# Kernel optimization log

Measured on AMD Instinct MI355X. Metric: run time of the kernel, lower is better.

Reference implementation:

```python
import jax, jax.numpy as jnp
import numpy as np

N_NODES = 50000
N_EDGES = 800000
IN_DIM = 128
HID = 128
N_GRAPHS = 1024


def gcn_conv(x, W, b, src, dst, n_nodes):
    # PyG GCNConv: add self-loops, symmetric normalization, aggregate at dst, then bias.
    loop = jnp.arange(n_nodes, dtype=src.dtype)
    s = jnp.concatenate([src, loop])
    d = jnp.concatenate([dst, loop])
    deg = jax.ops.segment_sum(jnp.ones_like(d, dtype=x.dtype), d, num_segments=n_nodes)
    dinv = jnp.where(deg > 0, deg ** -0.5, 0.0)
    norm = dinv[s] * dinv[d]                      # [E+N]
    h = x @ W                                     # [N, out]
    msg = h[s] * norm[:, None]                    # gather + scale
    out = jax.ops.segment_sum(msg, d, num_segments=n_nodes)  # scatter-add
    return out + b


def setup_inputs() -> dict:
    key = jax.random.key(0)
    ks = jax.random.split(key, 10)
    x = jax.random.normal(ks[0], (N_NODES, IN_DIM), dtype=jnp.float32)
    src = jax.random.randint(ks[1], (N_EDGES,), 0, N_NODES, dtype=jnp.int32)
    dst = jax.random.randint(ks[2], (N_EDGES,), 0, N_NODES, dtype=jnp.int32)
    batch = jnp.sort(jax.random.randint(ks[3], (N_NODES,), 0, N_GRAPHS, dtype=jnp.int32))
    sc1 = 1.0 / np.sqrt(IN_DIM)
    sc2 = 1.0 / np.sqrt(HID)
    W1 = jax.random.uniform(ks[4], (IN_DIM, HID), jnp.float32, -sc1, sc1)
    b1 = jnp.zeros((HID,), jnp.float32)
    W2 = jax.random.uniform(ks[5], (HID, HID), jnp.float32, -sc2, sc2)
    b2 = jnp.zeros((HID,), jnp.float32)
    Wlin = jax.random.uniform(ks[6], (HID, 1), jnp.float32, -sc2, sc2)
    blin = jnp.zeros((1,), jnp.float32)
    return {"x": x, "src": src, "dst": dst, "batch": batch, "n_graphs": N_GRAPHS,
            "W1": W1, "b1": b1, "W2": W2, "b2": b2, "Wlin": Wlin, "blin": blin}


def reference(x, src, dst, batch, n_graphs, W1, b1, W2, b2, Wlin, blin):
    n = x.shape[0]
    h = jax.nn.relu(gcn_conv(x, W1, b1, src, dst, n))
    h = jax.nn.relu(gcn_conv(h, W2, b2, src, dst, n))
    # global_mean_pool over graph assignment
    summed = jax.ops.segment_sum(h, batch, num_segments=n_graphs)
    cnt = jax.ops.segment_sum(jnp.ones((n,), h.dtype), batch, num_segments=n_graphs)
    pooled = summed / jnp.maximum(cnt, 1.0)[:, None]
    return (pooled @ Wlin + blin).reshape(-1)
```

## Files before the change

### kernel.cpp

```cpp
#include <hip/hip_runtime.h>
#include <hip/hip_bf16.h>

#define DIM 128
typedef unsigned int u32;

typedef __attribute__((ext_vector_type(8))) short bf16x8;
typedef __attribute__((ext_vector_type(4))) float f32x4;
typedef __attribute__((ext_vector_type(2))) float f32x2;

__device__ __forceinline__ u32 pack_bf16x2(float a, float b) {
    u32 ua = __float_as_uint(a), ub = __float_as_uint(b);
    ua = (ua + 0x7FFFu + ((ua >> 16) & 1u)) >> 16;
    ub = (ub + 0x7FFFu + ((ub >> 16) & 1u)) >> 16;
    return ua | (ub << 16);
}
__device__ __forceinline__ float2 unpack_bf16x2(u32 h) {
    return make_float2(__uint_as_float(h << 16), __uint_as_float(h & 0xFFFF0000u));
}

#if __has_builtin(__builtin_amdgcn_cvt_pk_f32_fp8) && __has_builtin(__builtin_amdgcn_cvt_pk_fp8_f32)
#define FP8_HW 1
#endif

__device__ __forceinline__ void dec4(float* d, u32 w) {
#ifdef FP8_HW
    f32x2 a = __builtin_amdgcn_cvt_pk_f32_fp8((int)w, false);
    f32x2 b = __builtin_amdgcn_cvt_pk_f32_fp8((int)w, true);
    d[0] = a.x; d[1] = a.y; d[2] = b.x; d[3] = b.y;
#else
    #pragma unroll
    for (int i = 0; i < 4; ++i) {
        u32 v = (w >> (8 * i)) & 0xFFu;
        u32 s = v >> 7, e = (v >> 3) & 15u, m = v & 7u;
        float nv = __uint_as_float((s << 31) | ((e + 120u) << 23) | (m << 20));
        float sv = (s ? -1.f : 1.f) * (float)m * 0.001953125f;
        d[i] = e ? nv : sv;
    }
#endif
}

#ifndef FP8_HW
__device__ __forceinline__ u32 enc_byte(float f) {
    u32 s = __float_as_uint(f) >> 31;
    float af = fminf(fabsf(f), 448.f);
    u32 b;
    if (af >= 0.015625f) {
        u32 m = __float_as_uint(af);
        m = m + 0x0007FFFFu + ((m >> 20) & 1u);
        u32 fe = (m >> 23) - 120u;
        if (fe > 15u) b = (15u << 3) | 6u;
        else          b = (fe << 3) | ((m >> 20) & 7u);
    } else {
        b = (u32)rintf(af * 512.f);
    }
    return b | (s << 7);
}
#endif

template<bool HI>
__device__ __forceinline__ u32 enc_pair(float a, float b, u32 old) {
#ifdef FP8_HW
    return (u32)__builtin_amdgcn_cvt_pk_fp8_f32(a, b, (int)old, HI);
#else
    u32 p = enc_byte(a) | (enc_byte(b) << 8);
    return HI ? ((old & 0x0000FFFFu) | (p << 16)) : ((old & 0xFFFF0000u) | p);
#endif
}

__device__ __forceinline__ void addrow16(float* acc, uint4 r) {
    float d[4];
    dec4(d, r.x);
    acc[0]  += d[0]; acc[1]  += d[1]; acc[2]  += d[2]; acc[3]  += d[3];
    dec4(d, r.y);
    acc[4]  += d[0]; acc[5]  += d[1]; acc[6]  += d[2]; acc[7]  += d[3];
    dec4(d, r.z);
    acc[8]  += d[0]; acc[9]  += d[1]; acc[10] += d[2]; acc[11] += d[3];
    dec4(d, r.w);
    acc[12] += d[0]; acc[13] += d[1]; acc[14] += d[2]; acc[15] += d[3];
}

__global__ void count_rank(int* __restrict__ deg, const int* __restrict__ dst,
                           int* __restrict__ rank, int* __restrict__ total, int E)
{
    int e = blockIdx.x * blockDim.x + threadIdx.x;
    if (e == 0) *total = 0;
    if (e < E) rank[e] = atomicAdd(&deg[dst[e]], 1);
}

__global__ __launch_bounds__(256) void alloc_offsets(
    const int* __restrict__ deg, int* __restrict__ start, int* __restrict__ endp,
    float* __restrict__ dinv, int* __restrict__ total,
    int* __restrict__ csr, int N,
    float* __restrict__ sums, float* __restrict__ cnt, int G,
    u32* __restrict__ B0, u32* __restrict__ B1)
{
    int i = blockIdx.x * blockDim.x + threadIdx.x;
    int lane = threadIdx.x & 63;
    if (i < G) { sums[i] = 0.f; cnt[i] = 0.f; }
    if (i < 32) {
        B0[(size_t)N * 32 + i] = 0u;
        B1[(size_t)N * 32 + i] = 0u;
    }
    int d  = (i < N) ? deg[i] : 0;
    int d4 = (d + 3) & ~3;
    int pre = d4;
    #pragma unroll
    for (int off = 1; off < 64; off <<= 1) {
        int v = __shfl_up(pre, off, 64);
        if (lane >= off) pre += v;
    }
    int waveTot = __shfl(pre, 63, 64);
    int base = 0;
    if (lane == 63) base = atomicAdd(total, waveTot);
    base = __shfl(base, 63, 64);
    if (i < N) {
        int st = base + pre - d4;
        start[i] = st;
        endp[i]  = st + d4;
        dinv[i]  = rsqrtf((float)(d + 1));
        for (int p = d; p < d4; ++p)
            csr[st + p] = N;
    }
}

__device__ __forceinline__ void gemm_body0(
    const float* __restrict__ X, const float* __restrict__ W,
    const float* __restrict__ dinv, u32* __restrict__ Y, int N,
    int tile0, int tstride)
{
    __shared__ u32   Abuf[16][68];
    __shared__ float Dbuf[16][132];

    const int t    = threadIdx.x;
    const int grp  = t >> 4;
    const int gl   = t & 15;
    const int lane = t & 63;
    const int wv   = t >> 6;
    const int lrow = lane & 15;
    const int lhi  = lane >> 4;

    bf16x8 bfr[2][4];
    {
        const float* wp = W + (size_t)(lhi * 8) * DIM + wv * 32 + lrow;
        #pragma unroll
        for (int nt = 0; nt < 2; ++nt)
            #pragma unroll
            for (int kc = 0; kc < 4; ++kc) {
                const float* p = wp + (size_t)(kc * 32) * DIM + nt * 16;
                union { u32 u[4]; bf16x8 v; } tmp;
                #pragma unroll
                for (int e = 0; e < 4; ++e)
                    tmp.u[e] = pack_bf16x2(p[(size_t)(2 * e) * DIM],
                                           p[(size_t)(2 * e + 1) * DIM]);
                bfr[nt][kc] = tmp.v;
            }
    }

    const int ntiles = (N + 15) >> 4;
    for (int tile = tile0; tile < ntiles; tile += tstride) {
        const int node = tile * 16 + grp;
        const bool valid = node < N;

        float4 a0 = make_float4(0.f, 0.f, 0.f, 0.f);
        float4 a1 = make_float4(0.f, 0.f, 0.f, 0.f);
        if (valid) {
            a0 = *(const float4*)&X[(size_t)node * DIM + gl * 8];
            a1 = *(const float4*)&X[(size_t)node * DIM + gl * 8 + 4];
        }
        uint4 pk;
        pk.x = pack_bf16x2(a0.x, a0.y);
        pk.y = pack_bf16x2(a0.z, a0.w);
        pk.z = pack_bf16x2(a1.x, a1.y);
        pk.w = pack_bf16x2(a1.z, a1.w);
        *(uint4*)&Abuf[grp][gl * 4] = pk;
        __syncthreads();

        f32x4 c0 = {0.f, 0.f, 0.f, 0.f};
        f32x4 c1 = {0.f, 0.f, 0.f, 0.f};
        #pragma unroll
        for (int kc = 0; kc < 4; ++kc) {
            bf16x8 afr = *(const bf16x8*)&Abuf[lrow][kc * 16 + lhi * 4];
            c0 = __builtin_amdgcn_mfma_f32_16x16x32_bf16(afr, bfr[0][kc], c0, 0, 0, 0);
            c1 = __builtin_amdgcn_mfma_f32_16x16x32_bf16(afr, bfr[1][kc], c1, 0, 0, 0);
        }
        #pragma unroll
        for (int r = 0; r < 4; ++r) {
            Dbuf[lhi * 4 + r][wv * 32 + lrow]      = c0[r];
            Dbuf[lhi * 4 + r][wv * 32 + 16 + lrow] = c1[r];
        }
        __syncthreads();

        if (valid) {
            float dnp = 16.f * dinv[node];
            float4 o0 = *(const float4*)&Dbuf[grp][gl * 8];
            float4 o1 = *(const float4*)&Dbuf[grp][gl * 8 + 4];
            u32 lo = enc_pair<false>(dnp * o0.x, dnp * o0.y, 0u);
            lo     = enc_pair<true >(dnp * o0.z, dnp * o0.w, lo);
            u32 hi = enc_pair<false>(dnp * o1.x, dnp * o1.y, 0u);
            hi     = enc_pair<true >(dnp * o1.z, dnp * o1.w, hi);
            *(uint2*)&Y[(size_t)node * 32 + gl * 2] = make_uint2(lo, hi);
        }
    }
}

__global__ __launch_bounds__(256) void scatter_gemm1(
    const float* __restrict__ x, const float* __restrict__ W1,
    const float* __restrict__ dinv, u32* __restrict__ Y, int N, int gblocks,
    const int* __restrict__ src, const int* __restrict__ dst,
    const int* __restrict__ rank, const int* __restrict__ start,
    int* __restrict__ csr, int E)
{
    if ((int)blockIdx.x < gblocks) {
        gemm_body0(x, W1, dinv, Y, N, blockIdx.x, gblocks);
    } else {
        int e = ((int)blockIdx.x - gblocks) * 256 + threadIdx.x;
        if (e < E) {
            int d = dst[e];
            csr[start[d] + rank[e]] = src[e];
        }
    }
}

__device__ __forceinline__ void gather_core16(
    const u32* __restrict__ Hl, const int* __restrict__ csr,
    int st, int en, float* acc)
{
    int j = st;
    if (j + 8 <= en) {
        int4 sa = *(const int4*)&csr[j];
        int4 sb = *(const int4*)&csr[j + 4];
        while (true) {
            int jn = j + 8;
            bool next8 = (jn + 8 <= en);
            int4 na, nb;
            if (next8) {
                na = *(const int4*)&csr[jn];
                nb = *(const int4*)&csr[jn + 4];
            }
            uint4 r0 = *(const uint4*)&Hl[(size_t)sa.x * 32];
            uint4 r1 = *(const uint4*)&Hl[(size_t)sa.y * 32];
            uint4 r2 = *(const uint4*)&Hl[(size_t)sa.z * 32];
            uint4 r3 = *(const uint4*)&Hl[(size_t)sa.w * 32];
            uint4 r4 = *(const uint4*)&Hl[(size_t)sb.x * 32];
            uint4 r5 = *(const uint4*)&Hl[(size_t)sb.y * 32];
            uint4 r6 = *(const uint4*)&Hl[(size_t)sb.z * 32];
            uint4 r7 = *(const uint4*)&Hl[(size_t)sb.w * 32];
            addrow16(acc, r0); addrow16(acc, r1);
            addrow16(acc, r2); addrow16(acc, r3);
            addrow16(acc, r4); addrow16(acc, r5);
            addrow16(acc, r6); addrow16(acc, r7);
            j = jn;
            if (!next8) break;
            sa = na; sb = nb;
        }
    }
    if (j < en) {
        int4 sa = *(const int4*)&csr[j];
        uint4 r0 = *(const uint4*)&Hl[(size_t)sa.x * 32];
        uint4 r1 = *(const uint4*)&Hl[(size_t)sa.y * 32];
        uint4 r2 = *(const uint4*)&Hl[(size_t)sa.z * 32];
        uint4 r3 = *(const uint4*)&Hl[(size_t)sa.w * 32];
        addrow16(acc, r0); addrow16(acc, r1);
        addrow16(acc, r2); addrow16(acc, r3);
    }
}

__global__ __launch_bounds__(256) void gather_gemm(
    const u32* __restrict__ H, u32* __restrict__ O,
    const int* __restrict__ csr, const int* __restrict__ start,
    const int* __restrict__ endp, const float* __restrict__ dinv, int N,
    const float* __restrict__ b1, const float* __restrict__ W2)
{
    __shared__ u32   Abuf[32][68];
    __shared__ float Dbuf[32][132];

    const int t    = threadIdx.x;
    const int grp  = t >> 3;
    const int gl   = t & 7;
    const int node = blockIdx.x * 32 + grp;
    const bool valid = node < N;

    const int lane = t & 63;
    const int wv   = t >> 6;
    const int lrow = lane & 15;
    const int lhi  = lane >> 4;

    bf16x8 bfr[2][4];
    {
        const float* wp = W2 + (size_t)(lhi * 8) * DIM + wv * 32 + lrow;
        #pragma unroll
        for (int nt = 0; nt < 2; ++nt)
            #pragma unroll
            for (int kc = 0; kc < 4; ++kc) {
                const float* p = wp + (size_t)(kc * 32) * DIM + nt * 16;
                union { u32 u[4]; bf16x8 v; } tmp;
                #pragma unroll
                for (int e = 0; e < 4; ++e)
                    tmp.u[e] = pack_bf16x2(p[(size_t)(2 * e) * DIM],
                                           p[(size_t)(2 * e + 1) * DIM]);
                bfr[nt][kc] = tmp.v;
            }
    }

    float acc[16];
    #pragma unroll
    for (int i = 0; i < 16; ++i) acc[i] = 0.f;
    float dn = 0.f;
    if (valid) {
        const u32* Hl = H + gl * 4;
        gather_core16(Hl, csr, start[node], endp[node], acc);
        addrow16(acc, *(const uint4*)&Hl[(size_t)node * 32]);
        dn = dinv[node] * 0.0625f;
    }

    {
        int f0 = gl * 16;
        float r[16];
        #pragma unroll
        for (int i = 0; i < 16; i += 4) {
            float4 bb = *(const float4*)&b1[f0 + i];
            r[i]     = fmaxf(fmaf(dn, acc[i],     bb.x), 0.f);
            r[i + 1] = fmaxf(fmaf(dn, acc[i + 1], bb.y), 0.f);
            r[i + 2] = fmaxf(fmaf(dn, acc[i + 2], bb.z), 0.f);
            r[i + 3] = fmaxf(fmaf(dn, acc[i + 3], bb.w), 0.f);
        }
        uint4 p0, p1;
        p0.x = pack_bf16x2(r[0],  r[1]);
        p0.y = pack_bf16x2(r[2],  r[3]);
        p0.z = pack_bf16x2(r[4],  r[5]);
        p0.w = pack_bf16x2(r[6],  r[7]);
        p1.x = pack_bf16x2(r[8],  r[9]);
        p1.y = pack_bf16x2(r[10], r[11]);
        p1.z = pack_bf16x2(r[12], r[13]);
        p1.w = pack_bf16x2(r[14], r[15]);
        *(uint4*)&Abuf[grp][gl * 8]     = p0;
        *(uint4*)&Abuf[grp][gl * 8 + 4] = p1;
    }
    __syncthreads();

    #pragma unroll
    for (int half = 0; half < 2; ++half) {
        f32x4 c0 = {0.f, 0.f, 0.f, 0.f};
        f32x4 c1 = {0.f, 0.f, 0.f, 0.f};
        #pragma unroll
        for (int kc = 0; kc < 4; ++kc) {
            bf16x8 afr = *(const bf16x8*)&Abuf[half * 16 + lrow][kc * 16 + lhi * 4];
            c0 = __builtin_amdgcn_mfma_f32_16x16x32_bf16(afr, bfr[0][kc], c0, 0, 0, 0);
            c1 = __builtin_amdgcn_mfma_f32_16x16x32_bf16(afr, bfr[1][kc], c1, 0, 0, 0);
        }
        #pragma unroll
        for (int r = 0; r < 4; ++r) {
            Dbuf[half * 16 + lhi * 4 + r][wv * 32 + lrow]      = c0[r];
            Dbuf[half * 16 + lhi * 4 + r][wv * 32 + 16 + lrow] = c1[r];
        }
    }
    __syncthreads();

    if (valid) {
        float dnp = 16.f * dinv[node];
        float o[16];
        #pragma unroll
        for (int i = 0; i < 16; ++i) o[i] = Dbuf[grp][gl * 16 + i];
        uint4 ov;
        ov.x = enc_pair<true>(dnp * o[2],  dnp * o[3],
               enc_pair<false>(dnp * o[0],  dnp * o[1],  0u));
        ov.y = enc_pair<true>(dnp * o[6],  dnp * o[7],
               enc_pair<false>(dnp * o[4],  dnp * o[5],  0u));
        ov.z = enc_pair<true>(dnp * o[10], dnp * o[11],
               enc_pair<false>(dnp * o[8],  dnp * o[9],  0u));
        ov.w = enc_pair<true>(dnp * o[14], dnp * o[15],
               enc_pair<false>(dnp * o[12], dnp * o[13], 0u));
        *(uint4*)&O[(size_t)node * 32 + gl * 4] = ov;
    }
}

__global__ __launch_bounds__(256) void gather_pool(
    const u32* __restrict__ H,
    const int* __restrict__ csr, const int* __restrict__ start,
    const int* __restrict__ endp, const float* __restrict__ dinv, int N,
    const float* __restrict__ b2, const float* __restrict__ wlin,
    const int* __restrict__ batch, float* __restrict__ sums, float* __restrict__ cnt)
{
    const int grp  = threadIdx.x >> 3;
    const int gl   = threadIdx.x & 7;
    const int node = blockIdx.x * 32 + grp;
    if (node >= N) return;

    float acc[16];
    #pragma unroll
    for (int i = 0; i < 16; ++i) acc[i] = 0.f;
    const u32* Hl = H + gl * 4;
    gather_core16(Hl, csr, start[node], endp[node], acc);
    addrow16(acc, *(const uint4*)&Hl[(size_t)node * 32]);
    float dn = dinv[node] * 0.0625f;

    int f0 = gl * 16;
    float v = 0.f;
    #pragma unroll
    for (int i = 0; i < 16; i += 4) {
        float4 bb = *(const float4*)&b2[f0 + i];
        float4 ww = *(const float4*)&wlin[f0 + i];
        v += fmaxf(fmaf(dn, acc[i],     bb.x), 0.f) * ww.x;
        v += fmaxf(fmaf(dn, acc[i + 1], bb.y), 0.f) * ww.y;
        v += fmaxf(fmaf(dn, acc[i + 2], bb.z), 0.f) * ww.z;
        v += fmaxf(fmaf(dn, acc[i + 3], bb.w), 0.f) * ww.w;
    }
    v += __shfl_xor(v, 1, 64);
    v += __shfl_xor(v, 2, 64);
    v += __shfl_xor(v, 4, 64);
    if (gl == 0) {
        int g = batch[node];
        unsafeAtomicAdd(&sums[g], v);
        unsafeAtomicAdd(&cnt[g], 1.0f);
    }
}

__global__ void final_kernel(const float* __restrict__ sums,
                             const float* __restrict__ cnt,
                             const float* __restrict__ blin,
                             float* __restrict__ out, int G)
{
    int g = blockIdx.x * blockDim.x + threadIdx.x;
    if (g < G) out[g] = sums[g] / fmaxf(cnt[g], 1.0f) + blin[0];
}


extern "C" void kernel_launch(void* const* d_in, const int* in_sizes, int n_in,
                              void* d_out, int out_size, void* d_ws, size_t ws_size,
                              hipStream_t stream)
{
    const float* x    = (const float*)d_in[0];
    const int*   src  = (const int*)d_in[1];
    const int*   dst  = (const int*)d_in[2];
    const int*   batch= (const int*)d_in[3];
    const float* W1   = (const float*)d_in[5];
    const float* b1   = (const float*)d_in[6];
    const float* W2   = (const float*)d_in[7];
    const float* b2   = (const float*)d_in[8];
    const float* wlin = (const float*)d_in[9];
    const float* blin = (const float*)d_in[10];
    float* out = (float*)d_out;

    const int N = in_sizes[0] / DIM;
    const int E = in_sizes[1];
    const int G = out_size;
    const size_t E_pad = (size_t)E + 4 * (size_t)N;

    u32*   B0    = (u32*)d_ws;
    u32*   B1    = B0 + (size_t)(N + 1) * 32;
    float* dinv  = (float*)(B1 + (size_t)(N + 1) * 32);
    float* sums  = dinv + N;
    float* cnt   = sums + G;
    int*   deg_c = (int*)(cnt + G);
    int*   start = deg_c + N;
    int*   endp  = start + N;
    int*   rank  = endp + N;
    int*   csr   = rank + E;
    int*   total = csr + E_pad;
    size_t need_bytes = ((size_t)(total + 1) - (size_t)d_ws);
    if (ws_size < need_bytes) return;

    const int eblocks  = (E + 255) / 256;
    const int g4blocks = (N + 15) / 16;
    const int g1blocks = g4blocks < 1024 ? g4blocks : 1024;
    const int g32blocks = (N + 31) / 32;

    (void)hipMemsetAsync(deg_c, 0, sizeof(int) * (size_t)N, stream);
    count_rank<<<eblocks, 256, 0, stream>>>(deg_c, dst, rank, total, E);
    alloc_offsets<<<(N + 255) / 256, 256, 0, stream>>>(deg_c, start, endp,
                                                       dinv, total, csr, N,
                                                       sums, cnt, G, B0, B1);
    scatter_gemm1<<<g1blocks + eblocks, 256, 0, stream>>>(x, W1, dinv, B0, N,
                                                          g1blocks, src, dst,
                                                          rank, start, csr, E);
    gather_gemm<<<g32blocks, 256, 0, stream>>>(B0, B1, csr, start, endp, dinv,
                                               N, b1, W2);
    gather_pool<<<g32blocks, 256, 0, stream>>>(B1, csr, start, endp, dinv, N,
                                               b2, wlin, batch, sums, cnt);
    final_kernel<<<(G + 255) / 256, 256, 0, stream>>>(sums, cnt, blin, out, G);
}
```

Measured before the change: 237.9 us.

## Sort nodes by degree for load-balanced gathers, pack CSR ranges, shrink pool blocks

Builds a degree histogram and scans it, then uses a counting sort to produce a permutation of nodes grouped by in-degree. The gather kernels walk nodes in that order so that nodes with similar degrees share a wavefront and divergence is reduced. Start and end offsets are packed into one int2 to save a load. gather_pool moves to 128-thread blocks of 16 nodes. In exchange the permuted order breaks spatial locality of output writes and of batch lookups, and adds an extra kernel launch plus atomic traffic.

```diff
diff --git a/kernel.cpp b/kernel.cpp
--- a/kernel.cpp
+++ b/kernel.cpp
@@ -80,19 +80,21 @@
 }
 
 __global__ void count_rank(int* __restrict__ deg, const int* __restrict__ dst,
-                           int* __restrict__ rank, int* __restrict__ total, int E)
+                           int* __restrict__ rank, int* __restrict__ total, int E,
+                           int* __restrict__ hist)
 {
     int e = blockIdx.x * blockDim.x + threadIdx.x;
     if (e == 0) *total = 0;
+    if (e < 256) hist[e] = 0;
     if (e < E) rank[e] = atomicAdd(&deg[dst[e]], 1);
 }
 
 __global__ __launch_bounds__(256) void alloc_offsets(
-    const int* __restrict__ deg, int* __restrict__ start, int* __restrict__ endp,
+    const int* __restrict__ deg, int2* __restrict__ rng,
     float* __restrict__ dinv, int* __restrict__ total,
     int* __restrict__ csr, int N,
     float* __restrict__ sums, float* __restrict__ cnt, int G,
-    u32* __restrict__ B0, u32* __restrict__ B1)
+    u32* __restrict__ B0, u32* __restrict__ B1, int* __restrict__ hist)
 {
     int i = blockIdx.x * blockDim.x + threadIdx.x;
     int lane = threadIdx.x & 63;
@@ -115,12 +117,29 @@
     base = __shfl(base, 63, 64);
     if (i < N) {
         int st = base + pre - d4;
-        start[i] = st;
-        endp[i]  = st + d4;
+        rng[i] = make_int2(st, st + d4);
         dinv[i]  = rsqrtf((float)(d + 1));
         for (int p = d; p < d4; ++p)
             csr[st + p] = N;
-    }
+        atomicAdd(&hist[d < 255 ? d : 255], 1);
+    }
+}
+
+__global__ __launch_bounds__(256) void scan_kernel(const int* __restrict__ hist,
+                                                   int* __restrict__ cursor)
+{
+    __shared__ int tmp[256];
+    int t = threadIdx.x;
+    int h = hist[t];
+    tmp[t] = h;
+    __syncthreads();
+    for (int off = 1; off < 256; off <<= 1) {
+        int v = (t >= off) ? tmp[t - off] : 0;
+        __syncthreads();
+        tmp[t] += v;
+        __syncthreads();
+    }
+    cursor[t] = tmp[t] - h;
 }
 
 __device__ __forceinline__ void gemm_body0(
@@ -207,16 +226,26 @@
     const float* __restrict__ x, const float* __restrict__ W1,
     const float* __restrict__ dinv, u32* __restrict__ Y, int N, int gblocks,
     const int* __restrict__ src, const int* __restrict__ dst,
-    const int* __restrict__ rank, const int* __restrict__ start,
-    int* __restrict__ csr, int E)
-{
-    if ((int)blockIdx.x < gblocks) {
-        gemm_body0(x, W1, dinv, Y, N, blockIdx.x, gblocks);
-    } else {
-        int e = ((int)blockIdx.x - gblocks) * 256 + threadIdx.x;
+    const int* __restrict__ rank, const int2* __restrict__ rng,
+    int* __restrict__ csr, int E, int eblocks,
+    const int* __restrict__ deg, int* __restrict__ cursor,
+    int* __restrict__ perm)
+{
+    int bid = (int)blockIdx.x;
+    if (bid < gblocks) {
+        gemm_body0(x, W1, dinv, Y, N, bid, gblocks);
+    } else if (bid < gblocks + eblocks) {
+        int e = (bid - gblocks) * 256 + threadIdx.x;
         if (e < E) {
             int d = dst[e];
-            csr[start[d] + rank[e]] = src[e];
+            csr[rng[d].x + rank[e]] = src[e];
+        }
+    } else {
+        int i = (bid - gblocks - eblocks) * 256 + threadIdx.x;
+        if (i < N) {
+            int k = deg[i]; if (k > 255) k = 255;
+            int slot = atomicAdd(&cursor[k], 1);
+            perm[slot] = i;
         }
     }
 }
@@ -267,9 +296,10 @@
 
 __global__ __launch_bounds__(256) void gather_gemm(
     const u32* __restrict__ H, u32* __restrict__ O,
-    const int* __restrict__ csr, const int* __restrict__ start,
-    const int* __restrict__ endp, const float* __restrict__ dinv, int N,
-    const float* __restrict__ b1, const float* __restrict__ W2)
+    const int* __restrict__ csr, const int2* __restrict__ rng,
+    const float* __restrict__ dinv, int N,
+    const float* __restrict__ b1, const float* __restrict__ W2,
+    const int* __restrict__ perm)
 {
     __shared__ u32   Abuf[32][68];
     __shared__ float Dbuf[32][132];
@@ -277,8 +307,8 @@
     const int t    = threadIdx.x;
     const int grp  = t >> 3;
     const int gl   = t & 7;
-    const int node = blockIdx.x * 32 + grp;
-    const bool valid = node < N;
+    const int idx  = blockIdx.x * 32 + grp;
+    const bool valid = idx < N;
 
     const int lane = t & 63;
     const int wv   = t >> 6;
@@ -306,9 +336,12 @@
     #pragma unroll
     for (int i = 0; i < 16; ++i) acc[i] = 0.f;
     float dn = 0.f;
+    int node = 0;
     if (valid) {
+        node = perm[idx];
         const u32* Hl = H + gl * 4;
-        gather_core16(Hl, csr, start[node], endp[node], acc);
+        int2 r = rng[node];
+        gather_core16(Hl, csr, r.x, r.y, acc);
         addrow16(acc, *(const uint4*)&Hl[(size_t)node * 32]);
         dn = dinv[node] * 0.0625f;
     }
@@ -374,23 +407,26 @@
     }
 }
 
-__global__ __launch_bounds__(256) void gather_pool(
+__global__ __launch_bounds__(128) void gather_pool(
     const u32* __restrict__ H,
-    const int* __restrict__ csr, const int* __restrict__ start,
-    const int* __restrict__ endp, const float* __restrict__ dinv, int N,
+    const int* __restrict__ csr, const int2* __restrict__ rng,
+    const float* __restrict__ dinv, int N,
     const float* __restrict__ b2, const float* __restrict__ wlin,
-    const int* __restrict__ batch, float* __restrict__ sums, float* __restrict__ cnt)
-{
-    const int grp  = threadIdx.x >> 3;
-    const int gl   = threadIdx.x & 7;
-    const int node = blockIdx.x * 32 + grp;
-    if (node >= N) return;
+    const int* __restrict__ batch, float* __restrict__ sums,
+    float* __restrict__ cnt, const int* __restrict__ perm)
+{
+    const int grp = threadIdx.x >> 3;
+    const int gl  = threadIdx.x & 7;
+    const int idx = blockIdx.x * 16 + grp;
+    if (idx >= N) return;
+    const int node = perm[idx];
 
     float acc[16];
     #pragma unroll
     for (int i = 0; i < 16; ++i) acc[i] = 0.f;
     const u32* Hl = H + gl * 4;
-    gather_core16(Hl, csr, start[node], endp[node], acc);
+    int2 r = rng[node];
+    gather_core16(Hl, csr, r.x, r.y, acc);
     addrow16(acc, *(const uint4*)&Hl[(size_t)node * 32]);
     float dn = dinv[node] * 0.0625f;
 
@@ -452,30 +488,33 @@
     float* sums  = dinv + N;
     float* cnt   = sums + G;
     int*   deg_c = (int*)(cnt + G);
-    int*   start = deg_c + N;
-    int*   endp  = start + N;
-    int*   rank  = endp + N;
+    int2*  rng   = (int2*)(deg_c + N);
+    int*   rank  = (int*)(rng + N);
     int*   csr   = rank + E;
-    int*   total = csr + E_pad;
+    int*   perm  = csr + E_pad;
+    int*   hist  = perm + N;
+    int*   cursor= hist + 256;
+    int*   total = cursor + 256;
     size_t need_bytes = ((size_t)(total + 1) - (size_t)d_ws);
     if (ws_size < need_bytes) return;
 
     const int eblocks  = (E + 255) / 256;
+    const int nblocks  = (N + 255) / 256;
     const int g4blocks = (N + 15) / 16;
     const int g1blocks = g4blocks < 1024 ? g4blocks : 1024;
     const int g32blocks = (N + 31) / 32;
 
     (void)hipMemsetAsync(deg_c, 0, sizeof(int) * (size_t)N, stream);
-    count_rank<<<eblocks, 256, 0, stream>>>(deg_c, dst, rank, total, E);
-    alloc_offsets<<<(N + 255) / 256, 256, 0, stream>>>(deg_c, start, endp,
-                                                       dinv, total, csr, N,
-                                                       sums, cnt, G, B0, B1);
-    scatter_gemm1<<<g1blocks + eblocks, 256, 0, stream>>>(x, W1, dinv, B0, N,
-                                                          g1blocks, src, dst,
-                                                          rank, start, csr, E);
-    gather_gemm<<<g32blocks, 256, 0, stream>>>(B0, B1, csr, start, endp, dinv,
-                                               N, b1, W2);
-    gather_pool<<<g32blocks, 256, 0, stream>>>(B1, csr, start, endp, dinv, N,
-                                               b2, wlin, batch, sums, cnt);
+    count_rank<<<eblocks, 256, 0, stream>>>(deg_c, dst, rank, total, E, hist);
+    alloc_offsets<<<nblocks, 256, 0, stream>>>(deg_c, rng, dinv, total, csr, N,
+                                               sums, cnt, G, B0, B1, hist);
+    scan_kernel<<<1, 256, 0, stream>>>(hist, cursor);
+    scatter_gemm1<<<g1blocks + eblocks + nblocks, 256, 0, stream>>>(
+        x, W1, dinv, B0, N, g1blocks, src, dst, rank, rng, csr, E, eblocks,
+        deg_c, cursor, perm);
+    gather_gemm<<<g32blocks, 256, 0, stream>>>(B0, B1, csr, rng, dinv,
+                                               N, b1, W2, perm);
+    gather_pool<<<g4blocks, 128, 0, stream>>>(B1, csr, rng, dinv, N,
+                                              b2, wlin, batch, sums, cnt, perm);
     final_kernel<<<(G + 255) / 256, 256, 0, stream>>>(sums, cnt, blin, out, G);
 }
```

After: 412.5 us. 1.73x slower.
